# Performance work log

Hardware: AMD Instinct MI355X
Metric: run time of the kernel (lower is better)

The kernel has to match this reference:

```python
import jax, jax.numpy as jnp
import numpy as np

N = 100000
F = 128
H = 128
E = 3200000


def setup_inputs() -> dict:
    key = jax.random.key(0)
    ks = jax.random.split(key, 12)
    s = 1.0 / np.sqrt(F)
    return {
        "x": jax.random.normal(ks[0], (N, F), jnp.float32),
        "edge_weight": jax.random.uniform(ks[1], (E,), jnp.float32),
        "p": jax.random.normal(ks[2], (F,), jnp.float32) * s,
        "w_ih": jax.random.normal(ks[3], (3 * F, F), jnp.float32) * s,
        "w_hh": jax.random.normal(ks[4], (3 * F, F), jnp.float32) * s,
        "b_ih": jax.random.normal(ks[5], (3 * F,), jnp.float32) * s,
        "b_hh": jax.random.normal(ks[6], (3 * F,), jnp.float32) * s,
        "w0": jax.random.normal(ks[7], (F, F), jnp.float32) * s,
        "w_lin": jax.random.normal(ks[8], (H, F), jnp.float32) * s,
        "b_lin": jax.random.normal(ks[9], (H,), jnp.float32) * s,
        "edge_index": jax.random.randint(ks[10], (2, E), 0, N, jnp.int64),
    }


def _evolve_gcnh(x, edge_index, edge_weight, p, w_ih, w_hh, b_ih, b_hh, w0):
    n_nodes, f = x.shape
    # --- TopKPooling: keep k = f nodes by learned projection score ---
    score = jnp.tanh((x @ p) / jnp.linalg.norm(p))  # [N]
    top_scores, idx = jax.lax.top_k(score, f)
    x_tilde = x[idx] * top_scores[:, None]  # [F, F]
    # --- single GRU step (batch=F, input=F): hidden state = GCN weight ---
    gi = x_tilde @ w_ih.T + b_ih  # [F, 3F]
    gh = w0 @ w_hh.T + b_hh       # [F, 3F]
    i_r, i_z, i_n = jnp.split(gi, 3, axis=-1)
    h_r, h_z, h_n = jnp.split(gh, 3, axis=-1)
    r = jax.nn.sigmoid(i_r + h_r)
    z = jax.nn.sigmoid(i_z + h_z)
    n = jnp.tanh(i_n + r * h_n)
    W = (1.0 - z) * n + z * w0  # evolved weight [F, F]
    # --- GCNConv with fixed W: sym-normalized sparse aggregation ---
    src, dst = edge_index[0], edge_index[1]
    loop = jnp.arange(n_nodes)
    src = jnp.concatenate([src, loop])
    dst = jnp.concatenate([dst, loop])
    ew = jnp.concatenate([edge_weight, jnp.ones((n_nodes,), x.dtype)])
    deg = jax.ops.segment_sum(ew, dst, num_segments=n_nodes)
    dinv = jnp.where(deg > 0, jax.lax.rsqrt(deg), 0.0)
    norm = dinv[src] * ew * dinv[dst]  # [E+N]
    xw = x @ W  # [N, F]
    out = jax.ops.segment_sum(norm[:, None] * xw[src], dst, num_segments=n_nodes)
    return out


def reference(x, edge_weight, p, w_ih, w_hh, b_ih, b_hh, w0, w_lin, b_lin, edge_index):
    h = _evolve_gcnh(x, edge_index, edge_weight, p, w_ih, w_hh, b_ih, b_hh, w0)
    h = jax.nn.relu(h)
    return h @ w_lin.T + b_lin
```

## Files before the change

kernel.cpp:

```cpp
#include <hip/hip_runtime.h>
#include <hip/hip_fp16.h>
#include <stdint.h>

#define FD 128
#define CAP 4096
#define PSH 8
#define NPART_MAX 512
#define NBLK1 1024
#define EBUF_MAX 4096

static inline size_t alignup256(size_t x) { return (x + 255) & ~(size_t)255; }

struct EdgeP { int s; float w; };

typedef __attribute__((ext_vector_type(4))) float f32x4;
typedef __attribute__((ext_vector_type(8))) short bf16x8;

__device__ __forceinline__ unsigned short f32_to_bf16(float f) {
  unsigned u = __float_as_uint(f);
  u += 0x7fffu + ((u >> 16) & 1u);
  return (unsigned short)(u >> 16);
}
__device__ __forceinline__ unsigned pack_bf16(float a, float b) {
  return ((unsigned)f32_to_bf16(b) << 16) | (unsigned)f32_to_bf16(a);
}
__device__ __forceinline__ unsigned pack_f16(float a, float b) {
  unsigned short ha = __half_as_ushort(__float2half_rn(a));
  unsigned short hb = __half_as_ushort(__float2half_rn(b));
  return ((unsigned)hb << 16) | (unsigned)ha;
}
__device__ __forceinline__ float f16lo(unsigned u) {
  return __half2float(__ushort_as_half((unsigned short)(u & 0xffffu)));
}
__device__ __forceinline__ float f16hi(unsigned u) {
  return __half2float(__ushort_as_half((unsigned short)(u >> 16)));
}
__device__ __forceinline__ unsigned mono32(float f) {
  unsigned u = __float_as_uint(f);
  return (u & 0x80000000u) ? ~u : (u | 0x80000000u);
}
__device__ __forceinline__ unsigned long long mono64(double d) {
  unsigned long long b = (unsigned long long)__double_as_longlong(d);
  return (b & 0x8000000000000000ULL) ? ~b : (b | 0x8000000000000000ULL);
}

__global__ void score_pack(const float* __restrict__ x, const float* __restrict__ p,
                           double* __restrict__ dvals, unsigned* __restrict__ hist,
                           unsigned short* __restrict__ xb, unsigned* __restrict__ cnt, int N)
{
  int gid = blockIdx.x * blockDim.x + threadIdx.x;
  if (gid == 0) *cnt = 0u;
  int wid = gid >> 6, lane = threadIdx.x & 63;
  int nw = (gridDim.x * blockDim.x) >> 6;
  double p0 = (double)p[lane * 2], p1 = (double)p[lane * 2 + 1];
  for (int n = wid; n < N; n += nw) {
    float2 xv = *(const float2*)(x + (size_t)n * FD + lane * 2);
    unsigned pk = pack_f16(xv.x, xv.y);
    *(unsigned*)(xb + (size_t)n * FD + lane * 2) = pk;
    double s = (double)xv.x * p0 + (double)xv.y * p1;
    #pragma unroll
    for (int o = 32; o > 0; o >>= 1) s += __shfl_down(s, o, 64);
    if (lane == 0) {
      dvals[n] = s;
      unsigned u = mono32((float)s);
      atomicAdd(&hist[u >> 16], 1u);
    }
  }
}

__global__ void find_thresh(const unsigned* __restrict__ hist, unsigned* __restrict__ Bthr)
{
  __shared__ unsigned part[1024];
  int t = threadIdx.x;
  unsigned s = 0;
  for (int i = 0; i < 64; i++) s += hist[t * 64 + i];
  part[t] = s;
  __syncthreads();
  if (t == 0) {
    unsigned cum = 0;
    int chunk = 1023;
    for (; chunk >= 0; chunk--) {
      if (cum + part[chunk] >= 128u) break;
      cum += part[chunk];
    }
    unsigned B = 0;
    if (chunk >= 0) {
      int b = chunk * 64 + 63;
      for (; b >= chunk * 64; b--) {
        cum += hist[b];
        if (cum >= 128u) break;
      }
      B = (unsigned)b;
    }
    *Bthr = B;
  }
}

__global__ void compact_kernel(const double* __restrict__ dvals, const unsigned* __restrict__ Bthr,
                               unsigned long long* __restrict__ ckey, unsigned* __restrict__ cidx,
                               unsigned* __restrict__ cnt, int N)
{
  int i = blockIdx.x * blockDim.x + threadIdx.x;
  if (i >= N) return;
  unsigned B = *Bthr;
  double d = dvals[i];
  unsigned u = mono32((float)d);
  if ((u >> 16) >= B) {
    unsigned pos = atomicAdd(cnt, 1u);
    if (pos < CAP) {
      ckey[pos] = ~mono64(d);
      cidx[pos] = (unsigned)i;
    }
  }
}

__global__ void topk_sort(const double* __restrict__ dvals, const float* __restrict__ p,
                          const unsigned* __restrict__ cnt,
                          const unsigned long long* __restrict__ ckey, const unsigned* __restrict__ cidx,
                          unsigned* __restrict__ sel_idx, float* __restrict__ sel_ts)
{
  __shared__ unsigned long long k[CAP];
  __shared__ unsigned id[CAP];
  __shared__ double red[128];
  __shared__ double pn_sh;
  int t = threadIdx.x;
  unsigned C = *cnt;
  if (C > CAP) C = CAP;
  int S = 128;
  while (S < (int)C) S <<= 1;
  for (int i = t; i < S; i += 1024) {
    if (i < (int)C) { k[i] = ckey[i]; id[i] = cidx[i]; }
    else            { k[i] = ~0ULL;   id[i] = 0xFFFFFFFFu; }
  }
  __syncthreads();
  for (int kk = 2; kk <= S; kk <<= 1) {
    for (int j = kk >> 1; j > 0; j >>= 1) {
      for (int i = t; i < S; i += 1024) {
        int q = i ^ j;
        if (q > i) {
          bool up = ((i & kk) == 0);
          bool g = (k[i] > k[q]) || (k[i] == k[q] && id[i] > id[q]);
          if (g == up) {
            unsigned long long tk = k[i]; k[i] = k[q]; k[q] = tk;
            unsigned ti = id[i]; id[i] = id[q]; id[q] = ti;
          }
        }
      }
      __syncthreads();
    }
  }
  if (t < 128) { double v = (double)p[t]; red[t] = v * v; }
  __syncthreads();
  if (t == 0) {
    double s = 0.0;
    for (int i = 0; i < 128; i++) s += red[i];
    pn_sh = sqrt(s);
  }
  __syncthreads();
  if (t < 128) {
    unsigned n = id[t];
    sel_idx[t] = n;
    sel_ts[t] = (float)tanh(dvals[n] / pn_sh);
  }
}

__global__ void transpose3(const float* __restrict__ w_ih, const float* __restrict__ w_hh,
                           const float* __restrict__ w_lin, float* __restrict__ w_ihT,
                           float* __restrict__ w_hhT, unsigned short* __restrict__ wlb)
{
  int b = blockIdx.x, c = threadIdx.x;
  if (b < 384)      w_ihT[(size_t)c * 384 + b]         = w_ih[(size_t)b * 128 + c];
  else if (b < 768) w_hhT[(size_t)c * 384 + (b - 384)] = w_hh[(size_t)(b - 384) * 128 + c];
  else              wlb[(size_t)(b - 768) * 128 + c]   = f32_to_bf16(w_lin[(size_t)(b - 768) * 128 + c]);
}

__global__ __launch_bounds__(384)
void gru_evolve(const float* __restrict__ x, const unsigned* __restrict__ sel_idx,
                const float* __restrict__ sel_ts,
                const float* __restrict__ w_ihT, const float* __restrict__ w_hhT,
                const float* __restrict__ b_ih, const float* __restrict__ b_hh,
                const float* __restrict__ w0, unsigned short* __restrict__ WbT)
{
  __shared__ float xt[FD], w0r[FD];
  __shared__ float gi[384], gh[384];
  int i = blockIdx.x, j = threadIdx.x;
  if (j < FD) {
    unsigned n = sel_idx[i];
    float ts = sel_ts[i];
    xt[j]  = x[(size_t)n * FD + j] * ts;
    w0r[j] = w0[i * FD + j];
  }
  __syncthreads();
  float gacc = b_ih[j], hacc = b_hh[j];
  for (int kx = 0; kx < FD; kx++) {
    float xv = xt[kx], hv = w0r[kx];
    gacc += xv * w_ihT[(size_t)kx * 384 + j];
    hacc += hv * w_hhT[(size_t)kx * 384 + j];
  }
  gi[j] = gacc;
  gh[j] = hacc;
  __syncthreads();
  if (j < FD) {
    float r = 1.f / (1.f + expf(-(gi[j] + gh[j])));
    float z = 1.f / (1.f + expf(-(gi[128 + j] + gh[128 + j])));
    float nn = tanhf(gi[256 + j] + r * gh[256 + j]);
    float wv = (1.f - z) * nn + z * w0r[j];
    WbT[(size_t)j * FD + i] = f32_to_bf16(wv);
  }
}

__global__ __launch_bounds__(1024)
void part_count(const int* __restrict__ dstA, unsigned* __restrict__ cnt,
                int E, int NPART)
{
  __shared__ unsigned lh[NPART_MAX];
  for (int i = threadIdx.x; i < NPART; i += 1024) lh[i] = 0;
  __syncthreads();
  int chunk = (E + gridDim.x - 1) / gridDim.x;
  int e0 = blockIdx.x * chunk;
  int e1 = e0 + chunk; if (e1 > E) e1 = E;
  for (int e = e0 + threadIdx.x; e < e1; e += 1024)
    atomicAdd(&lh[dstA[e] >> PSH], 1u);
  __syncthreads();
  for (int i = threadIdx.x; i < NPART; i += 1024)
    cnt[(size_t)i * NBLK1 + blockIdx.x] = lh[i];
}

__global__ __launch_bounds__(1024)
void scan_blocks(const unsigned* __restrict__ cnt, unsigned* __restrict__ basel,
                 unsigned* __restrict__ ptot)
{
  __shared__ unsigned s[NBLK1];
  int p = blockIdx.x, t = threadIdx.x;
  unsigned c = cnt[(size_t)p * NBLK1 + t];
  s[t] = c;
  __syncthreads();
  for (int ofs = 1; ofs < NBLK1; ofs <<= 1) {
    unsigned u = (t >= ofs) ? s[t - ofs] : 0u;
    __syncthreads();
    s[t] += u;
    __syncthreads();
  }
  basel[(size_t)p * NBLK1 + t] = s[t] - c;
  if (t == NBLK1 - 1) ptot[p] = s[t];
}

__global__ void scan_parts(const unsigned* __restrict__ ptot, int* __restrict__ poff,
                           int NPART, int E)
{
  __shared__ unsigned s[NPART_MAX];
  int t = threadIdx.x;
  unsigned c = (t < NPART) ? ptot[t] : 0u;
  s[t] = c;
  __syncthreads();
  for (int ofs = 1; ofs < NPART_MAX; ofs <<= 1) {
    unsigned u = (t >= ofs) ? s[t - ofs] : 0u;
    __syncthreads();
    s[t] += u;
    __syncthreads();
  }
  if (t < NPART) poff[t] = (int)(s[t] - c);
  if (t == 0) poff[NPART] = E;
}

__global__ __launch_bounds__(512)
void part_place(const int* __restrict__ srcA, const int* __restrict__ dstA,
                const float* __restrict__ ew, const int* __restrict__ poff,
                const unsigned* __restrict__ basel,
                unsigned long long* __restrict__ epk2, int E, int NPART)
{
  __shared__ unsigned long long ebuf[EBUF_MAX];
  __shared__ unsigned lcnt[NPART_MAX];
  __shared__ unsigned lsc[NPART_MAX];
  __shared__ unsigned lbase[NPART_MAX + 1];
  __shared__ unsigned cur[NPART_MAX];
  __shared__ int gbase[NPART_MAX];
  int b = blockIdx.x, t = threadIdx.x;
  int chunk = (E + gridDim.x - 1) / gridDim.x;
  int e0 = b * chunk;
  int e1 = e0 + chunk; if (e1 > E) e1 = E;
  int n = e1 - e0;

  lcnt[t] = 0;
  __syncthreads();
  for (int e = e0 + t; e < e1; e += 512)
    atomicAdd(&lcnt[dstA[e] >> PSH], 1u);
  __syncthreads();
  lsc[t] = lcnt[t];
  __syncthreads();
  for (int ofs = 1; ofs < NPART_MAX; ofs <<= 1) {
    unsigned u = (t >= ofs) ? lsc[t - ofs] : 0u;
    __syncthreads();
    lsc[t] += u;
    __syncthreads();
  }
  lbase[t] = lsc[t] - lcnt[t];
  if (t == NPART_MAX - 1) lbase[NPART_MAX] = lsc[t];
  cur[t] = lsc[t] - lcnt[t];
  gbase[t] = (t < NPART) ? (poff[t] + (int)basel[(size_t)t * NBLK1 + b]) : 0;
  __syncthreads();
  for (int e = e0 + t; e < e1; e += 512) {
    int d = dstA[e];
    int s = srcA[e];
    float w = ew[e];
    int p = d >> PSH;
    unsigned long long v = ((unsigned long long)__float_as_uint(w) << 32)
                         | ((unsigned long long)(unsigned)s << 8)
                         | (unsigned long long)(d & 255);
    unsigned pos = atomicAdd(&cur[p], 1u);
    ebuf[pos] = v;
  }
  __syncthreads();
  for (int j = t; j < n; j += 512) {
    int lo = 0, hi = NPART_MAX;
    while (hi - lo > 1) {
      int mid = (lo + hi) >> 1;
      if (lbase[mid] <= (unsigned)j) lo = mid; else hi = mid;
    }
    epk2[gbase[lo] + (j - (int)lbase[lo])] = ebuf[j];
  }
}

__global__ void part_csr(const int* __restrict__ poff, const unsigned long long* __restrict__ epk2,
                         EdgeP* __restrict__ epk_out, int* __restrict__ off,
                         float* __restrict__ dinv, int N, int NPART)
{
  int p = blockIdx.x;
  int beg = poff[p], end = poff[p + 1];
  int n0 = p << PSH;
  int nn = N - n0; if (nn > 256) nn = 256;
  __shared__ unsigned lcnt[256];
  __shared__ float ldeg[256];
  __shared__ unsigned lsc[256];
  int t = threadIdx.x;
  lcnt[t] = 0; ldeg[t] = 0.f;
  __syncthreads();
  for (int i = beg + t; i < end; i += 256) {
    unsigned long long v = epk2[i];
    int ln = (int)(v & 255u);
    float w = __uint_as_float((unsigned)(v >> 32));
    atomicAdd(&lcnt[ln], 1u);
    atomicAdd(&ldeg[ln], w);
  }
  __syncthreads();
  unsigned c = lcnt[t];
  lsc[t] = c;
  __syncthreads();
  for (int ofs = 1; ofs < 256; ofs <<= 1) {
    unsigned u = (t >= ofs) ? lsc[t - ofs] : 0u;
    __syncthreads();
    lsc[t] += u;
    __syncthreads();
  }
  unsigned excl = lsc[t] - c;
  if (t < nn) {
    off[n0 + t] = beg + (int)excl;
    dinv[n0 + t] = rsqrtf(ldeg[t] + 1.0f);
  }
  if (p == NPART - 1 && t == 0) off[N] = end;
  lcnt[t] = excl;
  __syncthreads();
  for (int i = beg + t; i < end; i += 256) {
    unsigned long long v = epk2[i];
    int ln = (int)(v & 255u);
    unsigned q = atomicAdd(&lcnt[ln], 1u);
    EdgeP ep;
    ep.s = (int)((v >> 8) & 0xFFFFFFu);
    ep.w = __uint_as_float((unsigned)(v >> 32));
    epk_out[beg + (int)q] = ep;
  }
}

__global__ __launch_bounds__(256)
void csr_gather4(const int* __restrict__ off, const EdgeP* __restrict__ epk,
                 const float* __restrict__ dinv, const unsigned short* __restrict__ xb,
                 unsigned short* __restrict__ aggb, int N)
{
  int gid = blockIdx.x * blockDim.x + threadIdx.x;
  int wid = gid >> 6, lane = threadIdx.x & 63;
  if (wid >= N) return;
  int g = lane >> 4, sub = lane & 15;
  int n = wid;
  int beg = off[n], end = off[n + 1];
  int cnt = end - beg;
  const EdgeP* ep_base = epk + beg;

  float di = dinv[n];
  uint4 xs4 = *(const uint4*)(xb + (size_t)n * FD + sub * 8);

  float acc[8];
  #pragma unroll
  for (int j = 0; j < 8; j++) acc[j] = 0.f;

  int nfull = cnt >> 4;
  int base = 0;
  for (int s16 = 0; s16 < nfull; s16++, base += 16) {
    uint2 ep[4];
    #pragma unroll
    for (int u = 0; u < 4; u++)
      ep[u] = *(const uint2*)(ep_base + base + u * 4 + g);
    float dv[4]; uint4 pv[4];
    #pragma unroll
    for (int u = 0; u < 4; u++) {
      int s = (int)ep[u].x;
      dv[u] = dinv[s];
      pv[u] = *(const uint4*)(xb + (size_t)s * FD + sub * 8);
    }
    #pragma unroll
    for (int u = 0; u < 4; u++) {
      float w = __uint_as_float(ep[u].y) * dv[u];
      acc[0] = fmaf(f16lo(pv[u].x), w, acc[0]); acc[1] = fmaf(f16hi(pv[u].x), w, acc[1]);
      acc[2] = fmaf(f16lo(pv[u].y), w, acc[2]); acc[3] = fmaf(f16hi(pv[u].y), w, acc[3]);
      acc[4] = fmaf(f16lo(pv[u].z), w, acc[4]); acc[5] = fmaf(f16hi(pv[u].z), w, acc[5]);
      acc[6] = fmaf(f16lo(pv[u].w), w, acc[6]); acc[7] = fmaf(f16hi(pv[u].w), w, acc[7]);
    }
  }
  if (base < cnt) {
    int last = cnt - 1;
    uint2 ep[4];
    #pragma unroll
    for (int u = 0; u < 4; u++) {
      int idx = base + u * 4 + g;
      int idc = idx < cnt ? idx : last;
      ep[u] = *(const uint2*)(ep_base + idc);
    }
    float dv[4]; uint4 pv[4];
    #pragma unroll
    for (int u = 0; u < 4; u++) {
      int s = (int)ep[u].x;
      dv[u] = dinv[s];
      pv[u] = *(const uint4*)(xb + (size_t)s * FD + sub * 8);
    }
    #pragma unroll
    for (int u = 0; u < 4; u++) {
      int idx = base + u * 4 + g;
      float w = (idx < cnt) ? __uint_as_float(ep[u].y) * dv[u] : 0.f;
      acc[0] = fmaf(f16lo(pv[u].x), w, acc[0]); acc[1] = fmaf(f16hi(pv[u].x), w, acc[1]);
      acc[2] = fmaf(f16lo(pv[u].y), w, acc[2]); acc[3] = fmaf(f16hi(pv[u].y), w, acc[3]);
      acc[4] = fmaf(f16lo(pv[u].z), w, acc[4]); acc[5] = fmaf(f16hi(pv[u].z), w, acc[5]);
      acc[6] = fmaf(f16lo(pv[u].w), w, acc[6]); acc[7] = fmaf(f16hi(pv[u].w), w, acc[7]);
    }
  }

  #pragma unroll
  for (int j = 0; j < 8; j++) {
    acc[j] += __shfl_xor(acc[j], 16, 64);
    acc[j] += __shfl_xor(acc[j], 32, 64);
  }
  if (g == 0) {
    float dii = di * di;
    uint4 o;
    o.x = pack_bf16(di * acc[0] + dii * f16lo(xs4.x), di * acc[1] + dii * f16hi(xs4.x));
    o.y = pack_bf16(di * acc[2] + dii * f16lo(xs4.y), di * acc[3] + dii * f16hi(xs4.y));
    o.z = pack_bf16(di * acc[4] + dii * f16lo(xs4.z), di * acc[5] + dii * f16hi(xs4.z));
    o.w = pack_bf16(di * acc[6] + dii * f16lo(xs4.w), di * acc[7] + dii * f16hi(xs4.w));
    *(uint4*)(aggb + (size_t)n * FD + sub * 8) = o;
  }
}

__global__ __launch_bounds__(256)
void gemm_mfma(const unsigned short* __restrict__ aggb, const unsigned short* __restrict__ WbT,
               const unsigned short* __restrict__ wlb, const float* __restrict__ bias,
               float* __restrict__ C, int nrows)
{
  __shared__ unsigned short hs[64][136];
  int tid = threadIdx.x;
  int wv = tid >> 6, lane = tid & 63;
  int row16 = lane & 15;
  int kgrp = lane >> 4;
  int r0 = blockIdx.x * 64;
  int arow = r0 + wv * 16 + row16;
  bool rowok = arow < nrows;

  f32x4 acc[8];
  #pragma unroll
  for (int t = 0; t < 8; t++) acc[t] = (f32x4){0.f, 0.f, 0.f, 0.f};

  #pragma unroll
  for (int ks = 0; ks < 4; ks++) {
    int k = ks * 32 + kgrp * 8;
    bf16x8 a;
    if (rowok) a = *(const bf16x8*)(aggb + (size_t)arow * FD + k);
    else       a = (bf16x8){0, 0, 0, 0, 0, 0, 0, 0};
    #pragma unroll
    for (int t = 0; t < 8; t++) {
      int col = t * 16 + row16;
      bf16x8 b = *(const bf16x8*)(WbT + (size_t)col * FD + k);
      acc[t] = __builtin_amdgcn_mfma_f32_16x16x32_bf16(a, b, acc[t], 0, 0, 0);
    }
  }
  #pragma unroll
  for (int t = 0; t < 8; t++) {
    int col = t * 16 + row16;
    #pragma unroll
    for (int r = 0; r < 4; r++) {
      int row_l = wv * 16 + kgrp * 4 + r;
      hs[row_l][col] = f32_to_bf16(fmaxf(acc[t][r], 0.f));
    }
  }
  __syncthreads();

  f32x4 acc2[8];
  #pragma unroll
  for (int t = 0; t < 8; t++) acc2[t] = (f32x4){0.f, 0.f, 0.f, 0.f};
  #pragma unroll
  for (int ks = 0; ks < 4; ks++) {
    int k = ks * 32 + kgrp * 8;
    bf16x8 a = *(const bf16x8*)(&hs[wv * 16 + row16][k]);
    #pragma unroll
    for (int t = 0; t < 8; t++) {
      int col = t * 16 + row16;
      bf16x8 b = *(const bf16x8*)(wlb + (size_t)col * FD + k);
      acc2[t] = __builtin_amdgcn_mfma_f32_16x16x32_bf16(a, b, acc2[t], 0, 0, 0);
    }
  }
  #pragma unroll
  for (int t = 0; t < 8; t++) {
    int col = t * 16 + row16;
    float bl = bias[col];
    #pragma unroll
    for (int r = 0; r < 4; r++) {
      int row = r0 + wv * 16 + kgrp * 4 + r;
      if (row < nrows) C[(size_t)row * FD + col] = acc2[t][r] + bl;
    }
  }
}

extern "C" void kernel_launch(void* const* d_in, const int* in_sizes, int n_in,
                              void* d_out, int out_size, void* d_ws, size_t ws_size,
                              hipStream_t stream)
{
  const float* x     = (const float*)d_in[0];
  const float* ew    = (const float*)d_in[1];
  const float* p     = (const float*)d_in[2];
  const float* w_ih  = (const float*)d_in[3];
  const float* w_hh  = (const float*)d_in[4];
  const float* b_ih  = (const float*)d_in[5];
  const float* b_hh  = (const float*)d_in[6];
  const float* w0    = (const float*)d_in[7];
  const float* w_lin = (const float*)d_in[8];
  const float* b_lin = (const float*)d_in[9];
  const int*   eidx  = (const int*)d_in[10];

  int N = in_sizes[0] / FD;
  int E = in_sizes[1];
  int NPART = (N + 255) >> PSH;
  const int* srcA = eidx;
  const int* dstA = eidx + E;

  char* base = (char*)d_ws;
  size_t off_ws = 0;
  auto take = [&](size_t bytes) -> void* {
    void* ptr = base + off_ws;
    off_ws = alignup256(off_ws + bytes);
    return ptr;
  };
  double* dvals = (double*)take((size_t)N * 8);
  unsigned* hist = (unsigned*)take(65536u * 4);
  unsigned* cnt = (unsigned*)take(4);
  unsigned* Bthr = (unsigned*)take(4);
  unsigned long long* ckey = (unsigned long long*)take((size_t)CAP * 8);
  unsigned* cidx = (unsigned*)take((size_t)CAP * 4);
  unsigned* sel_idx = (unsigned*)take(128 * 4);
  float* sel_ts = (float*)take(128 * 4);
  unsigned short* WbT = (unsigned short*)take(FD * FD * 2);
  unsigned short* wlb = (unsigned short*)take(FD * FD * 2);
  float* w_ihT = (float*)take(3 * FD * FD * 4);
  float* w_hhT = (float*)take(3 * FD * FD * 4);
  float* dinv = (float*)take((size_t)N * 4);
  unsigned* pcnt = (unsigned*)take((size_t)NPART_MAX * NBLK1 * 4);
  unsigned* basel = (unsigned*)take((size_t)NPART_MAX * NBLK1 * 4);
  unsigned* ptot = (unsigned*)take((size_t)NPART_MAX * 4);
  int* poff = (int*)take(((size_t)NPART_MAX + 1) * 4);
  int* off = (int*)take(((size_t)N + 1) * 4);
  unsigned long long* epk2 = (unsigned long long*)take((size_t)E * 8);
  EdgeP* epk_b = (EdgeP*)take((size_t)E * 8);
  unsigned short* xb = (unsigned short*)take((size_t)N * FD * 2);
  unsigned short* aggb = (unsigned short*)take((size_t)N * FD * 2);
  float* out1 = (float*)d_out;

  hipMemsetAsync(hist, 0, 65536u * 4, stream);

  score_pack<<<2048, 256, 0, stream>>>(x, p, dvals, hist, xb, cnt, N);
  find_thresh<<<1, 1024, 0, stream>>>(hist, Bthr);
  compact_kernel<<<(N + 255) / 256, 256, 0, stream>>>(dvals, Bthr, ckey, cidx, cnt, N);
  topk_sort<<<1, 1024, 0, stream>>>(dvals, p, cnt, ckey, cidx, sel_idx, sel_ts);
  transpose3<<<896, 128, 0, stream>>>(w_ih, w_hh, w_lin, w_ihT, w_hhT, wlb);
  gru_evolve<<<128, 384, 0, stream>>>(x, sel_idx, sel_ts, w_ihT, w_hhT, b_ih, b_hh, w0, WbT);

  part_count<<<NBLK1, 1024, 0, stream>>>(dstA, pcnt, E, NPART);
  scan_blocks<<<NPART, NBLK1, 0, stream>>>(pcnt, basel, ptot);
  scan_parts<<<1, NPART_MAX, 0, stream>>>(ptot, poff, NPART, E);
  part_place<<<NBLK1, 512, 0, stream>>>(srcA, dstA, ew, poff, basel, epk2, E, NPART);
  part_csr<<<NPART, 256, 0, stream>>>(poff, epk2, epk_b, off, dinv, N, NPART);

  csr_gather4<<<(N * 64 + 255) / 256, 256, 0, stream>>>(off, epk_b, dinv, xb, aggb, N);
  gemm_mfma<<<(N + 63) / 64, 256, 0, stream>>>(aggb, WbT, wlb, b_lin, out1, N);
}
```

Baseline: 400.4 us.

## Merge independent pipeline stages into shared launches via block-index dispatch

Cuts the launch count from 13 kernels to 6. Independent stages (score/pack, edge partition count, weight transpose; threshold and partition scan; compaction and edge placement; top-k sort and CSR build; GRU and gather) now share one launch each, with blocks routed by block index. The partition offset scan is folded into consumers, which recompute prefix sums of ptot on the fly and drop the poff buffer. The aim is to remove launch gaps and let small serial kernels overlap with large bandwidth-bound ones, at the cost of smaller block sizes for some stages (sort at 256 threads) and redundant prefix sums.

```diff
diff --git a/kernel.cpp b/kernel.cpp
--- a/kernel.cpp
+++ b/kernel.cpp
@@ -8,6 +8,8 @@
 #define NPART_MAX 512
 #define NBLK1 1024
 #define EBUF_MAX 4096
+#define SCORE_BLKS 2048
+#define TRANS_BLKS 448
 
 static inline size_t alignup256(size_t x) { return (x + 255) & ~(size_t)255; }
 
@@ -44,417 +46,425 @@
   return (b & 0x8000000000000000ULL) ? ~b : (b | 0x8000000000000000ULL);
 }
 
-__global__ void score_pack(const float* __restrict__ x, const float* __restrict__ p,
-                           double* __restrict__ dvals, unsigned* __restrict__ hist,
-                           unsigned short* __restrict__ xb, unsigned* __restrict__ cnt, int N)
+__global__ __launch_bounds__(256)
+void k_front(const float* __restrict__ x, const float* __restrict__ pvec,
+             double* __restrict__ dvals, unsigned* __restrict__ hist,
+             unsigned short* __restrict__ xb, unsigned* __restrict__ cnt, int N,
+             const int* __restrict__ dstA, unsigned* __restrict__ pcnt, int E, int NPART,
+             const float* __restrict__ w_ih, const float* __restrict__ w_hh,
+             const float* __restrict__ w_lin, float* __restrict__ w_ihT,
+             float* __restrict__ w_hhT, unsigned short* __restrict__ wlb)
 {
-  int gid = blockIdx.x * blockDim.x + threadIdx.x;
-  if (gid == 0) *cnt = 0u;
-  int wid = gid >> 6, lane = threadIdx.x & 63;
-  int nw = (gridDim.x * blockDim.x) >> 6;
-  double p0 = (double)p[lane * 2], p1 = (double)p[lane * 2 + 1];
-  for (int n = wid; n < N; n += nw) {
-    float2 xv = *(const float2*)(x + (size_t)n * FD + lane * 2);
-    unsigned pk = pack_f16(xv.x, xv.y);
-    *(unsigned*)(xb + (size_t)n * FD + lane * 2) = pk;
-    double s = (double)xv.x * p0 + (double)xv.y * p1;
-    #pragma unroll
-    for (int o = 32; o > 0; o >>= 1) s += __shfl_down(s, o, 64);
-    if (lane == 0) {
-      dvals[n] = s;
-      unsigned u = mono32((float)s);
-      atomicAdd(&hist[u >> 16], 1u);
-    }
-  }
-}
-
-__global__ void find_thresh(const unsigned* __restrict__ hist, unsigned* __restrict__ Bthr)
+  int b = blockIdx.x, t = threadIdx.x;
+  if (b < SCORE_BLKS) {
+    int gid = b * 256 + t;
+    if (gid == 0) *cnt = 0u;
+    int wid = gid >> 6, lane = t & 63;
+    const int nw = (SCORE_BLKS * 256) >> 6;
+    double p0 = (double)pvec[lane * 2], p1 = (double)pvec[lane * 2 + 1];
+    for (int n = wid; n < N; n += nw) {
+      float2 xv = *(const float2*)(x + (size_t)n * FD + lane * 2);
+      unsigned pk = pack_f16(xv.x, xv.y);
+      *(unsigned*)(xb + (size_t)n * FD + lane * 2) = pk;
+      double s = (double)xv.x * p0 + (double)xv.y * p1;
+      #pragma unroll
+      for (int o = 32; o > 0; o >>= 1) s += __shfl_down(s, o, 64);
+      if (lane == 0) {
+        dvals[n] = s;
+        unsigned u = mono32((float)s);
+        atomicAdd(&hist[u >> 16], 1u);
+      }
+    }
+  } else if (b < SCORE_BLKS + NBLK1) {
+    __shared__ unsigned lh[NPART_MAX];
+    int bid = b - SCORE_BLKS;
+    for (int i = t; i < NPART; i += 256) lh[i] = 0;
+    __syncthreads();
+    int chunk = (E + NBLK1 - 1) / NBLK1;
+    int e0 = bid * chunk;
+    int e1 = e0 + chunk; if (e1 > E) e1 = E;
+    for (int e = e0 + t; e < e1; e += 256)
+      atomicAdd(&lh[dstA[e] >> PSH], 1u);
+    __syncthreads();
+    for (int i = t; i < NPART; i += 256)
+      pcnt[(size_t)i * NBLK1 + bid] = lh[i];
+  } else {
+    int vb = (b - SCORE_BLKS - NBLK1) * 2 + (t >> 7);
+    int c = t & 127;
+    if (vb < 384)      w_ihT[(size_t)c * 384 + vb]         = w_ih[(size_t)vb * 128 + c];
+    else if (vb < 768) w_hhT[(size_t)c * 384 + (vb - 384)] = w_hh[(size_t)(vb - 384) * 128 + c];
+    else               wlb[(size_t)(vb - 768) * 128 + c]   = f32_to_bf16(w_lin[(size_t)(vb - 768) * 128 + c]);
+  }
+}
+
+__global__ __launch_bounds__(1024)
+void k_mid1(const unsigned* __restrict__ hist, unsigned* __restrict__ Bthr,
+            const unsigned* __restrict__ pcnt, unsigned* __restrict__ basel,
+            unsigned* __restrict__ ptot)
 {
-  __shared__ unsigned part[1024];
   int t = threadIdx.x;
-  unsigned s = 0;
-  for (int i = 0; i < 64; i++) s += hist[t * 64 + i];
-  part[t] = s;
-  __syncthreads();
-  if (t == 0) {
-    unsigned cum = 0;
-    int chunk = 1023;
-    for (; chunk >= 0; chunk--) {
-      if (cum + part[chunk] >= 128u) break;
-      cum += part[chunk];
-    }
-    unsigned B = 0;
-    if (chunk >= 0) {
-      int b = chunk * 64 + 63;
-      for (; b >= chunk * 64; b--) {
-        cum += hist[b];
-        if (cum >= 128u) break;
-      }
-      B = (unsigned)b;
-    }
-    *Bthr = B;
-  }
-}
-
-__global__ void compact_kernel(const double* __restrict__ dvals, const unsigned* __restrict__ Bthr,
-                               unsigned long long* __restrict__ ckey, unsigned* __restrict__ cidx,
-                               unsigned* __restrict__ cnt, int N)
+  if (blockIdx.x == 0) {
+    __shared__ unsigned part[1024];
+    unsigned s = 0;
+    for (int i = 0; i < 64; i++) s += hist[t * 64 + i];
+    part[t] = s;
+    __syncthreads();
+    if (t == 0) {
+      unsigned cum = 0;
+      int chunk = 1023;
+      for (; chunk >= 0; chunk--) {
+        if (cum + part[chunk] >= 128u) break;
+        cum += part[chunk];
+      }
+      unsigned B = 0;
+      if (chunk >= 0) {
+        int b = chunk * 64 + 63;
+        for (; b >= chunk * 64; b--) {
+          cum += hist[b];
+          if (cum >= 128u) break;
+        }
+        B = (unsigned)b;
+      }
+      *Bthr = B;
+    }
+  } else {
+    __shared__ unsigned s[NBLK1];
+    int p = blockIdx.x - 1;
+    unsigned c = pcnt[(size_t)p * NBLK1 + t];
+    s[t] = c;
+    __syncthreads();
+    for (int ofs = 1; ofs < NBLK1; ofs <<= 1) {
+      unsigned u = (t >= ofs) ? s[t - ofs] : 0u;
+      __syncthreads();
+      s[t] += u;
+      __syncthreads();
+    }
+    basel[(size_t)p * NBLK1 + t] = s[t] - c;
+    if (t == NBLK1 - 1) ptot[p] = s[t];
+  }
+}
+
+__global__ __launch_bounds__(512)
+void k_mid2(const int* __restrict__ srcA, const int* __restrict__ dstA,
+            const float* __restrict__ ew, const unsigned* __restrict__ ptot,
+            const unsigned* __restrict__ basel, unsigned long long* __restrict__ epk2,
+            int E, int NPART,
+            const double* __restrict__ dvals, const unsigned* __restrict__ Bthr,
+            unsigned long long* __restrict__ ckey, unsigned* __restrict__ cidx,
+            unsigned* __restrict__ cnt, int N)
 {
-  int i = blockIdx.x * blockDim.x + threadIdx.x;
-  if (i >= N) return;
-  unsigned B = *Bthr;
-  double d = dvals[i];
-  unsigned u = mono32((float)d);
-  if ((u >> 16) >= B) {
-    unsigned pos = atomicAdd(cnt, 1u);
-    if (pos < CAP) {
-      ckey[pos] = ~mono64(d);
-      cidx[pos] = (unsigned)i;
-    }
-  }
-}
-
-__global__ void topk_sort(const double* __restrict__ dvals, const float* __restrict__ p,
-                          const unsigned* __restrict__ cnt,
-                          const unsigned long long* __restrict__ ckey, const unsigned* __restrict__ cidx,
-                          unsigned* __restrict__ sel_idx, float* __restrict__ sel_ts)
+  int t = threadIdx.x;
+  if (blockIdx.x < NBLK1) {
+    __shared__ unsigned long long ebuf[EBUF_MAX];
+    __shared__ unsigned lcnt[NPART_MAX];
+    __shared__ unsigned lsc[NPART_MAX];
+    __shared__ unsigned psc[NPART_MAX];
+    __shared__ unsigned lbase[NPART_MAX + 1];
+    __shared__ unsigned cur[NPART_MAX];
+    __shared__ int gbase[NPART_MAX];
+    int b = blockIdx.x;
+    int chunk = (E + NBLK1 - 1) / NBLK1;
+    int e0 = b * chunk;
+    int e1 = e0 + chunk; if (e1 > E) e1 = E;
+    int n = e1 - e0;
+
+    lcnt[t] = 0;
+    unsigned pt = (t < NPART) ? ptot[t] : 0u;
+    __syncthreads();
+    for (int e = e0 + t; e < e1; e += 512)
+      atomicAdd(&lcnt[dstA[e] >> PSH], 1u);
+    __syncthreads();
+    lsc[t] = lcnt[t];
+    psc[t] = pt;
+    __syncthreads();
+    for (int ofs = 1; ofs < NPART_MAX; ofs <<= 1) {
+      unsigned u1 = (t >= ofs) ? lsc[t - ofs] : 0u;
+      unsigned u2 = (t >= ofs) ? psc[t - ofs] : 0u;
+      __syncthreads();
+      lsc[t] += u1;
+      psc[t] += u2;
+      __syncthreads();
+    }
+    lbase[t] = lsc[t] - lcnt[t];
+    if (t == NPART_MAX - 1) lbase[NPART_MAX] = lsc[t];
+    cur[t] = lsc[t] - lcnt[t];
+    gbase[t] = (t < NPART) ? ((int)(psc[t] - pt) + (int)basel[(size_t)t * NBLK1 + b]) : 0;
+    __syncthreads();
+    for (int e = e0 + t; e < e1; e += 512) {
+      int d = dstA[e];
+      int s = srcA[e];
+      float w = ew[e];
+      int p = d >> PSH;
+      unsigned long long v = ((unsigned long long)__float_as_uint(w) << 32)
+                           | ((unsigned long long)(unsigned)s << 8)
+                           | (unsigned long long)(d & 255);
+      unsigned pos = atomicAdd(&cur[p], 1u);
+      ebuf[pos] = v;
+    }
+    __syncthreads();
+    for (int j = t; j < n; j += 512) {
+      int lo = 0, hi = NPART_MAX;
+      while (hi - lo > 1) {
+        int mid = (lo + hi) >> 1;
+        if (lbase[mid] <= (unsigned)j) lo = mid; else hi = mid;
+      }
+      epk2[gbase[lo] + (j - (int)lbase[lo])] = ebuf[j];
+    }
+  } else {
+    int i = (blockIdx.x - NBLK1) * 512 + t;
+    if (i >= N) return;
+    unsigned B = *Bthr;
+    double d = dvals[i];
+    unsigned u = mono32((float)d);
+    if ((u >> 16) >= B) {
+      unsigned pos = atomicAdd(cnt, 1u);
+      if (pos < CAP) {
+        ckey[pos] = ~mono64(d);
+        cidx[pos] = (unsigned)i;
+      }
+    }
+  }
+}
+
+__global__ __launch_bounds__(256)
+void k_mid3(const double* __restrict__ dvals, const float* __restrict__ pvec,
+            const unsigned* __restrict__ cnt,
+            const unsigned long long* __restrict__ ckey, const unsigned* __restrict__ cidx,
+            unsigned* __restrict__ sel_idx, float* __restrict__ sel_ts,
+            const unsigned* __restrict__ ptot, const unsigned long long* __restrict__ epk2,
+            EdgeP* __restrict__ epk_out, int* __restrict__ off,
+            float* __restrict__ dinv, int N, int NPART)
 {
-  __shared__ unsigned long long k[CAP];
-  __shared__ unsigned id[CAP];
-  __shared__ double red[128];
-  __shared__ double pn_sh;
   int t = threadIdx.x;
-  unsigned C = *cnt;
-  if (C > CAP) C = CAP;
-  int S = 128;
-  while (S < (int)C) S <<= 1;
-  for (int i = t; i < S; i += 1024) {
-    if (i < (int)C) { k[i] = ckey[i]; id[i] = cidx[i]; }
-    else            { k[i] = ~0ULL;   id[i] = 0xFFFFFFFFu; }
-  }
-  __syncthreads();
-  for (int kk = 2; kk <= S; kk <<= 1) {
-    for (int j = kk >> 1; j > 0; j >>= 1) {
-      for (int i = t; i < S; i += 1024) {
-        int q = i ^ j;
-        if (q > i) {
-          bool up = ((i & kk) == 0);
-          bool g = (k[i] > k[q]) || (k[i] == k[q] && id[i] > id[q]);
-          if (g == up) {
-            unsigned long long tk = k[i]; k[i] = k[q]; k[q] = tk;
-            unsigned ti = id[i]; id[i] = id[q]; id[q] = ti;
+  if (blockIdx.x == 0) {
+    __shared__ unsigned long long k[CAP];
+    __shared__ unsigned id[CAP];
+    __shared__ double red[128];
+    __shared__ double pn_sh;
+    unsigned C = *cnt;
+    if (C > CAP) C = CAP;
+    int S = 128;
+    while (S < (int)C) S <<= 1;
+    for (int i = t; i < S; i += 256) {
+      if (i < (int)C) { k[i] = ckey[i]; id[i] = cidx[i]; }
+      else            { k[i] = ~0ULL;   id[i] = 0xFFFFFFFFu; }
+    }
+    __syncthreads();
+    for (int kk = 2; kk <= S; kk <<= 1) {
+      for (int j = kk >> 1; j > 0; j >>= 1) {
+        for (int i = t; i < S; i += 256) {
+          int q = i ^ j;
+          if (q > i) {
+            bool up = ((i & kk) == 0);
+            bool g = (k[i] > k[q]) || (k[i] == k[q] && id[i] > id[q]);
+            if (g == up) {
+              unsigned long long tk = k[i]; k[i] = k[q]; k[q] = tk;
+              unsigned ti = id[i]; id[i] = id[q]; id[q] = ti;
+            }
           }
         }
-      }
+        __syncthreads();
+      }
+    }
+    if (t < 128) { double v = (double)pvec[t]; red[t] = v * v; }
+    __syncthreads();
+    if (t == 0) {
+      double s = 0.0;
+      for (int i = 0; i < 128; i++) s += red[i];
+      pn_sh = sqrt(s);
+    }
+    __syncthreads();
+    if (t < 128) {
+      unsigned n = id[t];
+      sel_idx[t] = n;
+      sel_ts[t] = (float)tanh(dvals[n] / pn_sh);
+    }
+  } else {
+    int p = blockIdx.x - 1;
+    __shared__ unsigned rsum[256];
+    unsigned a = 0;
+    for (int i = t; i < p; i += 256) a += ptot[i];
+    rsum[t] = a;
+    __syncthreads();
+    for (int ofs = 128; ofs > 0; ofs >>= 1) {
+      if (t < ofs) rsum[t] += rsum[t + ofs];
       __syncthreads();
     }
-  }
-  if (t < 128) { double v = (double)p[t]; red[t] = v * v; }
-  __syncthreads();
-  if (t == 0) {
-    double s = 0.0;
-    for (int i = 0; i < 128; i++) s += red[i];
-    pn_sh = sqrt(s);
-  }
-  __syncthreads();
-  if (t < 128) {
-    unsigned n = id[t];
-    sel_idx[t] = n;
-    sel_ts[t] = (float)tanh(dvals[n] / pn_sh);
-  }
-}
-
-__global__ void transpose3(const float* __restrict__ w_ih, const float* __restrict__ w_hh,
-                           const float* __restrict__ w_lin, float* __restrict__ w_ihT,
-                           float* __restrict__ w_hhT, unsigned short* __restrict__ wlb)
+    int beg = (int)rsum[0];
+    int end = beg + (int)ptot[p];
+
+    int n0 = p << PSH;
+    int nn = N - n0; if (nn > 256) nn = 256;
+    __shared__ unsigned lcnt[256];
+    __shared__ float ldeg[256];
+    __shared__ unsigned lsc[256];
+    lcnt[t] = 0; ldeg[t] = 0.f;
+    __syncthreads();
+    for (int i = beg + t; i < end; i += 256) {
+      unsigned long long v = epk2[i];
+      int ln = (int)(v & 255u);
+      float w = __uint_as_float((unsigned)(v >> 32));
+      atomicAdd(&lcnt[ln], 1u);
+      atomicAdd(&ldeg[ln], w);
+    }
+    __syncthreads();
+    unsigned c = lcnt[t];
+    lsc[t] = c;
+    __syncthreads();
+    for (int ofs = 1; ofs < 256; ofs <<= 1) {
+      unsigned u = (t >= ofs) ? lsc[t - ofs] : 0u;
+      __syncthreads();
+      lsc[t] += u;
+      __syncthreads();
+    }
+    unsigned excl = lsc[t] - c;
+    if (t < nn) {
+      off[n0 + t] = beg + (int)excl;
+      dinv[n0 + t] = rsqrtf(ldeg[t] + 1.0f);
+    }
+    if (p == NPART - 1 && t == 0) off[N] = end;
+    lcnt[t] = excl;
+    __syncthreads();
+    for (int i = beg + t; i < end; i += 256) {
+      unsigned long long v = epk2[i];
+      int ln = (int)(v & 255u);
+      unsigned q = atomicAdd(&lcnt[ln], 1u);
+      EdgeP ep;
+      ep.s = (int)((v >> 8) & 0xFFFFFFu);
+      ep.w = __uint_as_float((unsigned)(v >> 32));
+      epk_out[beg + (int)q] = ep;
+    }
+  }
+}
+
+__global__ __launch_bounds__(256)
+void k_gg(const float* __restrict__ x, const unsigned* __restrict__ sel_idx,
+          const float* __restrict__ sel_ts,
+          const float* __restrict__ w_ihT, const float* __restrict__ w_hhT,
+          const float* __restrict__ b_ih, const float* __restrict__ b_hh,
+          const float* __restrict__ w0, unsigned short* __restrict__ WbT,
+          const int* __restrict__ off, const EdgeP* __restrict__ epk,
+          const float* __restrict__ dinv, const unsigned short* __restrict__ xb,
+          unsigned short* __restrict__ aggb, int N)
 {
-  int b = blockIdx.x, c = threadIdx.x;
-  if (b < 384)      w_ihT[(size_t)c * 384 + b]         = w_ih[(size_t)b * 128 + c];
-  else if (b < 768) w_hhT[(size_t)c * 384 + (b - 384)] = w_hh[(size_t)(b - 384) * 128 + c];
-  else              wlb[(size_t)(b - 768) * 128 + c]   = f32_to_bf16(w_lin[(size_t)(b - 768) * 128 + c]);
-}
-
-__global__ __launch_bounds__(384)
-void gru_evolve(const float* __restrict__ x, const unsigned* __restrict__ sel_idx,
-                const float* __restrict__ sel_ts,
-                const float* __restrict__ w_ihT, const float* __restrict__ w_hhT,
-                const float* __restrict__ b_ih, const float* __restrict__ b_hh,
-                const float* __restrict__ w0, unsigned short* __restrict__ WbT)
-{
-  __shared__ float xt[FD], w0r[FD];
-  __shared__ float gi[384], gh[384];
-  int i = blockIdx.x, j = threadIdx.x;
-  if (j < FD) {
-    unsigned n = sel_idx[i];
-    float ts = sel_ts[i];
-    xt[j]  = x[(size_t)n * FD + j] * ts;
-    w0r[j] = w0[i * FD + j];
-  }
-  __syncthreads();
-  float gacc = b_ih[j], hacc = b_hh[j];
-  for (int kx = 0; kx < FD; kx++) {
-    float xv = xt[kx], hv = w0r[kx];
-    gacc += xv * w_ihT[(size_t)kx * 384 + j];
-    hacc += hv * w_hhT[(size_t)kx * 384 + j];
-  }
-  gi[j] = gacc;
-  gh[j] = hacc;
-  __syncthreads();
-  if (j < FD) {
-    float r = 1.f / (1.f + expf(-(gi[j] + gh[j])));
-    float z = 1.f / (1.f + expf(-(gi[128 + j] + gh[128 + j])));
-    float nn = tanhf(gi[256 + j] + r * gh[256 + j]);
-    float wv = (1.f - z) * nn + z * w0r[j];
-    WbT[(size_t)j * FD + i] = f32_to_bf16(wv);
-  }
-}
-
-__global__ __launch_bounds__(1024)
-void part_count(const int* __restrict__ dstA, unsigned* __restrict__ cnt,
-                int E, int NPART)
-{
-  __shared__ unsigned lh[NPART_MAX];
-  for (int i = threadIdx.x; i < NPART; i += 1024) lh[i] = 0;
-  __syncthreads();
-  int chunk = (E + gridDim.x - 1) / gridDim.x;
-  int e0 = blockIdx.x * chunk;
-  int e1 = e0 + chunk; if (e1 > E) e1 = E;
-  for (int e = e0 + threadIdx.x; e < e1; e += 1024)
-    atomicAdd(&lh[dstA[e] >> PSH], 1u);
-  __syncthreads();
-  for (int i = threadIdx.x; i < NPART; i += 1024)
-    cnt[(size_t)i * NBLK1 + blockIdx.x] = lh[i];
-}
-
-__global__ __launch_bounds__(1024)
-void scan_blocks(const unsigned* __restrict__ cnt, unsigned* __restrict__ basel,
-                 unsigned* __restrict__ ptot)
-{
-  __shared__ unsigned s[NBLK1];
-  int p = blockIdx.x, t = threadIdx.x;
-  unsigned c = cnt[(size_t)p * NBLK1 + t];
-  s[t] = c;
-  __syncthreads();
-  for (int ofs = 1; ofs < NBLK1; ofs <<= 1) {
-    unsigned u = (t >= ofs) ? s[t - ofs] : 0u;
-    __syncthreads();
-    s[t] += u;
-    __syncthreads();
-  }
-  basel[(size_t)p * NBLK1 + t] = s[t] - c;
-  if (t == NBLK1 - 1) ptot[p] = s[t];
-}
-
-__global__ void scan_parts(const unsigned* __restrict__ ptot, int* __restrict__ poff,
-                           int NPART, int E)
-{
-  __shared__ unsigned s[NPART_MAX];
   int t = threadIdx.x;
-  unsigned c = (t < NPART) ? ptot[t] : 0u;
-  s[t] = c;
-  __syncthreads();
-  for (int ofs = 1; ofs < NPART_MAX; ofs <<= 1) {
-    unsigned u = (t >= ofs) ? s[t - ofs] : 0u;
-    __syncthreads();
-    s[t] += u;
-    __syncthreads();
-  }
-  if (t < NPART) poff[t] = (int)(s[t] - c);
-  if (t == 0) poff[NPART] = E;
-}
-
-__global__ __launch_bounds__(512)
-void part_place(const int* __restrict__ srcA, const int* __restrict__ dstA,
-                const float* __restrict__ ew, const int* __restrict__ poff,
-                const unsigned* __restrict__ basel,
-                unsigned long long* __restrict__ epk2, int E, int NPART)
-{
-  __shared__ unsigned long long ebuf[EBUF_MAX];
-  __shared__ unsigned lcnt[NPART_MAX];
-  __shared__ unsigned lsc[NPART_MAX];
-  __shared__ unsigned lbase[NPART_MAX + 1];
-  __shared__ unsigned cur[NPART_MAX];
-  __shared__ int gbase[NPART_MAX];
-  int b = blockIdx.x, t = threadIdx.x;
-  int chunk = (E + gridDim.x - 1) / gridDim.x;
-  int e0 = b * chunk;
-  int e1 = e0 + chunk; if (e1 > E) e1 = E;
-  int n = e1 - e0;
-
-  lcnt[t] = 0;
-  __syncthreads();
-  for (int e = e0 + t; e < e1; e += 512)
-    atomicAdd(&lcnt[dstA[e] >> PSH], 1u);
-  __syncthreads();
-  lsc[t] = lcnt[t];
-  __syncthreads();
-  for (int ofs = 1; ofs < NPART_MAX; ofs <<= 1) {
-    unsigned u = (t >= ofs) ? lsc[t - ofs] : 0u;
-    __syncthreads();
-    lsc[t] += u;
-    __syncthreads();
-  }
-  lbase[t] = lsc[t] - lcnt[t];
-  if (t == NPART_MAX - 1) lbase[NPART_MAX] = lsc[t];
-  cur[t] = lsc[t] - lcnt[t];
-  gbase[t] = (t < NPART) ? (poff[t] + (int)basel[(size_t)t * NBLK1 + b]) : 0;
-  __syncthreads();
-  for (int e = e0 + t; e < e1; e += 512) {
-    int d = dstA[e];
-    int s = srcA[e];
-    float w = ew[e];
-    int p = d >> PSH;
-    unsigned long long v = ((unsigned long long)__float_as_uint(w) << 32)
-                         | ((unsigned long long)(unsigned)s << 8)
-                         | (unsigned long long)(d & 255);
-    unsigned pos = atomicAdd(&cur[p], 1u);
-    ebuf[pos] = v;
-  }
-  __syncthreads();
-  for (int j = t; j < n; j += 512) {
-    int lo = 0, hi = NPART_MAX;
-    while (hi - lo > 1) {
-      int mid = (lo + hi) >> 1;
-      if (lbase[mid] <= (unsigned)j) lo = mid; else hi = mid;
-    }
-    epk2[gbase[lo] + (j - (int)lbase[lo])] = ebuf[j];
-  }
-}
-
-__global__ void part_csr(const int* __restrict__ poff, const unsigned long long* __restrict__ epk2,
-                         EdgeP* __restrict__ epk_out, int* __restrict__ off,
-                         float* __restrict__ dinv, int N, int NPART)
-{
-  int p = blockIdx.x;
-  int beg = poff[p], end = poff[p + 1];
-  int n0 = p << PSH;
-  int nn = N - n0; if (nn > 256) nn = 256;
-  __shared__ unsigned lcnt[256];
-  __shared__ float ldeg[256];
-  __shared__ unsigned lsc[256];
-  int t = threadIdx.x;
-  lcnt[t] = 0; ldeg[t] = 0.f;
-  __syncthreads();
-  for (int i = beg + t; i < end; i += 256) {
-    unsigned long long v = epk2[i];
-    int ln = (int)(v & 255u);
-    float w = __uint_as_float((unsigned)(v >> 32));
-    atomicAdd(&lcnt[ln], 1u);
-    atomicAdd(&ldeg[ln], w);
-  }
-  __syncthreads();
-  unsigned c = lcnt[t];
-  lsc[t] = c;
-  __syncthreads();
-  for (int ofs = 1; ofs < 256; ofs <<= 1) {
-    unsigned u = (t >= ofs) ? lsc[t - ofs] : 0u;
-    __syncthreads();
-    lsc[t] += u;
-    __syncthreads();
-  }
-  unsigned excl = lsc[t] - c;
-  if (t < nn) {
-    off[n0 + t] = beg + (int)excl;
-    dinv[n0 + t] = rsqrtf(ldeg[t] + 1.0f);
-  }
-  if (p == NPART - 1 && t == 0) off[N] = end;
-  lcnt[t] = excl;
-  __syncthreads();
-  for (int i = beg + t; i < end; i += 256) {
-    unsigned long long v = epk2[i];
-    int ln = (int)(v & 255u);
-    unsigned q = atomicAdd(&lcnt[ln], 1u);
-    EdgeP ep;
-    ep.s = (int)((v >> 8) & 0xFFFFFFu);
-    ep.w = __uint_as_float((unsigned)(v >> 32));
-    epk_out[beg + (int)q] = ep;
-  }
-}
-
-__global__ __launch_bounds__(256)
-void csr_gather4(const int* __restrict__ off, const EdgeP* __restrict__ epk,
-                 const float* __restrict__ dinv, const unsigned short* __restrict__ xb,
-                 unsigned short* __restrict__ aggb, int N)
-{
-  int gid = blockIdx.x * blockDim.x + threadIdx.x;
-  int wid = gid >> 6, lane = threadIdx.x & 63;
-  if (wid >= N) return;
-  int g = lane >> 4, sub = lane & 15;
-  int n = wid;
-  int beg = off[n], end = off[n + 1];
-  int cnt = end - beg;
-  const EdgeP* ep_base = epk + beg;
-
-  float di = dinv[n];
-  uint4 xs4 = *(const uint4*)(xb + (size_t)n * FD + sub * 8);
-
-  float acc[8];
-  #pragma unroll
-  for (int j = 0; j < 8; j++) acc[j] = 0.f;
-
-  int nfull = cnt >> 4;
-  int base = 0;
-  for (int s16 = 0; s16 < nfull; s16++, base += 16) {
-    uint2 ep[4];
+  if (blockIdx.x < 128) {
+    __shared__ float xt[FD], w0r[FD];
+    __shared__ float gi[384], gh[384];
+    int i = blockIdx.x;
+    if (t < FD) {
+      unsigned n = sel_idx[i];
+      float ts = sel_ts[i];
+      xt[t]  = x[(size_t)n * FD + t] * ts;
+      w0r[t] = w0[i * FD + t];
+    }
+    __syncthreads();
+    bool has2 = t < 128;
+    float ga0 = b_ih[t], ha0 = b_hh[t];
+    float ga1 = 0.f, ha1 = 0.f;
+    if (has2) { ga1 = b_ih[256 + t]; ha1 = b_hh[256 + t]; }
+    for (int kx = 0; kx < FD; kx++) {
+      float xv = xt[kx], hv = w0r[kx];
+      const float* wi = w_ihT + (size_t)kx * 384;
+      const float* wh = w_hhT + (size_t)kx * 384;
+      ga0 += xv * wi[t];
+      ha0 += hv * wh[t];
+      if (has2) {
+        ga1 += xv * wi[256 + t];
+        ha1 += hv * wh[256 + t];
+      }
+    }
+    gi[t] = ga0; gh[t] = ha0;
+    if (has2) { gi[256 + t] = ga1; gh[256 + t] = ha1; }
+    __syncthreads();
+    if (t < FD) {
+      float r = 1.f / (1.f + expf(-(gi[t] + gh[t])));
+      float z = 1.f / (1.f + expf(-(gi[128 + t] + gh[128 + t])));
+      float nn = tanhf(gi[256 + t] + r * gh[256 + t]);
+      float wv = (1.f - z) * nn + z * w0r[t];
+      WbT[(size_t)t * FD + i] = f32_to_bf16(wv);
+    }
+  } else {
+    int gid = (blockIdx.x - 128) * 256 + t;
+    int wid = gid >> 6, lane = t & 63;
+    if (wid >= N) return;
+    int g = lane >> 4, sub = lane & 15;
+    int n = wid;
+    int beg = off[n], end = off[n + 1];
+    int cnt = end - beg;
+    const EdgeP* ep_base = epk + beg;
+
+    float di = dinv[n];
+    uint4 xs4 = *(const uint4*)(xb + (size_t)n * FD + sub * 8);
+
+    float acc[8];
     #pragma unroll
-    for (int u = 0; u < 4; u++)
-      ep[u] = *(const uint2*)(ep_base + base + u * 4 + g);
-    float dv[4]; uint4 pv[4];
+    for (int j = 0; j < 8; j++) acc[j] = 0.f;
+
+    int nfull = cnt >> 4;
+    int base = 0;
+    for (int s16 = 0; s16 < nfull; s16++, base += 16) {
+      uint2 ep[4];
+      #pragma unroll
+      for (int u = 0; u < 4; u++)
+        ep[u] = *(const uint2*)(ep_base + base + u * 4 + g);
+      float dv[4]; uint4 pv[4];
+      #pragma unroll
+      for (int u = 0; u < 4; u++) {
+        int s = (int)ep[u].x;
+        dv[u] = dinv[s];
+        pv[u] = *(const uint4*)(xb + (size_t)s * FD + sub * 8);
+      }
+      #pragma unroll
+      for (int u = 0; u < 4; u++) {
+        float w = __uint_as_float(ep[u].y) * dv[u];
+        acc[0] = fmaf(f16lo(pv[u].x), w, acc[0]); acc[1] = fmaf(f16hi(pv[u].x), w, acc[1]);
+        acc[2] = fmaf(f16lo(pv[u].y), w, acc[2]); acc[3] = fmaf(f16hi(pv[u].y), w, acc[3]);
+        acc[4] = fmaf(f16lo(pv[u].z), w, acc[4]); acc[5] = fmaf(f16hi(pv[u].z), w, acc[5]);
+        acc[6] = fmaf(f16lo(pv[u].w), w, acc[6]); acc[7] = fmaf(f16hi(pv[u].w), w, acc[7]);
+      }
+    }
+    if (base < cnt) {
+      int last = cnt - 1;
+      uint2 ep[4];
+      #pragma unroll
+      for (int u = 0; u < 4; u++) {
+        int idx = base + u * 4 + g;
+        int idc = idx < cnt ? idx : last;
+        ep[u] = *(const uint2*)(ep_base + idc);
+      }
+      float dv[4]; uint4 pv[4];
+      #pragma unroll
+      for (int u = 0; u < 4; u++) {
+        int s = (int)ep[u].x;
+        dv[u] = dinv[s];
+        pv[u] = *(const uint4*)(xb + (size_t)s * FD + sub * 8);
+      }
+      #pragma unroll
+      for (int u = 0; u < 4; u++) {
+        int idx = base + u * 4 + g;
+        float w = (idx < cnt) ? __uint_as_float(ep[u].y) * dv[u] : 0.f;
+        acc[0] = fmaf(f16lo(pv[u].x), w, acc[0]); acc[1] = fmaf(f16hi(pv[u].x), w, acc[1]);
+        acc[2] = fmaf(f16lo(pv[u].y), w, acc[2]); acc[3] = fmaf(f16hi(pv[u].y), w, acc[3]);
+        acc[4] = fmaf(f16lo(pv[u].z), w, acc[4]); acc[5] = fmaf(f16hi(pv[u].z), w, acc[5]);
+        acc[6] = fmaf(f16lo(pv[u].w), w, acc[6]); acc[7] = fmaf(f16hi(pv[u].w), w, acc[7]);
+      }
+    }
+
     #pragma unroll
-    for (int u = 0; u < 4; u++) {
-      int s = (int)ep[u].x;
-      dv[u] = dinv[s];
-      pv[u] = *(const uint4*)(xb + (size_t)s * FD + sub * 8);
-    }
-    #pragma unroll
-    for (int u = 0; u < 4; u++) {
-      float w = __uint_as_float(ep[u].y) * dv[u];
-      acc[0] = fmaf(f16lo(pv[u].x), w, acc[0]); acc[1] = fmaf(f16hi(pv[u].x), w, acc[1]);
-      acc[2] = fmaf(f16lo(pv[u].y), w, acc[2]); acc[3] = fmaf(f16hi(pv[u].y), w, acc[3]);
-      acc[4] = fmaf(f16lo(pv[u].z), w, acc[4]); acc[5] = fmaf(f16hi(pv[u].z), w, acc[5]);
-      acc[6] = fmaf(f16lo(pv[u].w), w, acc[6]); acc[7] = fmaf(f16hi(pv[u].w), w, acc[7]);
-    }
-  }
-  if (base < cnt) {
-    int last = cnt - 1;
-    uint2 ep[4];
-    #pragma unroll
-    for (int u = 0; u < 4; u++) {
-      int idx = base + u * 4 + g;
-      int idc = idx < cnt ? idx : last;
-      ep[u] = *(const uint2*)(ep_base + idc);
-    }
-    float dv[4]; uint4 pv[4];
-    #pragma unroll
-    for (int u = 0; u < 4; u++) {
-      int s = (int)ep[u].x;
-      dv[u] = dinv[s];
-      pv[u] = *(const uint4*)(xb + (size_t)s * FD + sub * 8);
-    }
-    #pragma unroll
-    for (int u = 0; u < 4; u++) {
-      int idx = base + u * 4 + g;
-      float w = (idx < cnt) ? __uint_as_float(ep[u].y) * dv[u] : 0.f;
-      acc[0] = fmaf(f16lo(pv[u].x), w, acc[0]); acc[1] = fmaf(f16hi(pv[u].x), w, acc[1]);
-      acc[2] = fmaf(f16lo(pv[u].y), w, acc[2]); acc[3] = fmaf(f16hi(pv[u].y), w, acc[3]);
-      acc[4] = fmaf(f16lo(pv[u].z), w, acc[4]); acc[5] = fmaf(f16hi(pv[u].z), w, acc[5]);
-      acc[6] = fmaf(f16lo(pv[u].w), w, acc[6]); acc[7] = fmaf(f16hi(pv[u].w), w, acc[7]);
-    }
-  }
-
-  #pragma unroll
-  for (int j = 0; j < 8; j++) {
-    acc[j] += __shfl_xor(acc[j], 16, 64);
-    acc[j] += __shfl_xor(acc[j], 32, 64);
-  }
-  if (g == 0) {
-    float dii = di * di;
-    uint4 o;
-    o.x = pack_bf16(di * acc[0] + dii * f16lo(xs4.x), di * acc[1] + dii * f16hi(xs4.x));
-    o.y = pack_bf16(di * acc[2] + dii * f16lo(xs4.y), di * acc[3] + dii * f16hi(xs4.y));
-    o.z = pack_bf16(di * acc[4] + dii * f16lo(xs4.z), di * acc[5] + dii * f16hi(xs4.z));
-    o.w = pack_bf16(di * acc[6] + dii * f16lo(xs4.w), di * acc[7] + dii * f16hi(xs4.w));
-    *(uint4*)(aggb + (size_t)n * FD + sub * 8) = o;
+    for (int j = 0; j < 8; j++) {
+      acc[j] += __shfl_xor(acc[j], 16, 64);
+      acc[j] += __shfl_xor(acc[j], 32, 64);
+    }
+    if (g == 0) {
+      float dii = di * di;
+      uint4 o;
+      o.x = pack_bf16(di * acc[0] + dii * f16lo(xs4.x), di * acc[1] + dii * f16hi(xs4.x));
+      o.y = pack_bf16(di * acc[2] + dii * f16lo(xs4.y), di * acc[3] + dii * f16hi(xs4.y));
+      o.z = pack_bf16(di * acc[4] + dii * f16lo(xs4.z), di * acc[5] + dii * f16hi(xs4.z));
+      o.w = pack_bf16(di * acc[6] + dii * f16lo(xs4.w), di * acc[7] + dii * f16hi(xs4.w));
+      *(uint4*)(aggb + (size_t)n * FD + sub * 8) = o;
+    }
   }
 }
 
@@ -532,7 +542,7 @@
 {
   const float* x     = (const float*)d_in[0];
   const float* ew    = (const float*)d_in[1];
-  const float* p     = (const float*)d_in[2];
+  const float* pvec  = (const float*)d_in[2];
   const float* w_ih  = (const float*)d_in[3];
   const float* w_hh  = (const float*)d_in[4];
   const float* b_ih  = (const float*)d_in[5];
@@ -571,7 +581,6 @@
   unsigned* pcnt = (unsigned*)take((size_t)NPART_MAX * NBLK1 * 4);
   unsigned* basel = (unsigned*)take((size_t)NPART_MAX * NBLK1 * 4);
   unsigned* ptot = (unsigned*)take((size_t)NPART_MAX * 4);
-  int* poff = (int*)take(((size_t)NPART_MAX + 1) * 4);
   int* off = (int*)take(((size_t)N + 1) * 4);
   unsigned long long* epk2 = (unsigned long long*)take((size_t)E * 8);
   EdgeP* epk_b = (EdgeP*)take((size_t)E * 8);
@@ -581,19 +590,18 @@
 
   hipMemsetAsync(hist, 0, 65536u * 4, stream);
 
-  score_pack<<<2048, 256, 0, stream>>>(x, p, dvals, hist, xb, cnt, N);
-  find_thresh<<<1, 1024, 0, stream>>>(hist, Bthr);
-  compact_kernel<<<(N + 255) / 256, 256, 0, stream>>>(dvals, Bthr, ckey, cidx, cnt, N);
-  topk_sort<<<1, 1024, 0, stream>>>(dvals, p, cnt, ckey, cidx, sel_idx, sel_ts);
-  transpose3<<<896, 128, 0, stream>>>(w_ih, w_hh, w_lin, w_ihT, w_hhT, wlb);
-  gru_evolve<<<128, 384, 0, stream>>>(x, sel_idx, sel_ts, w_ihT, w_hhT, b_ih, b_hh, w0, WbT);
-
-  part_count<<<NBLK1, 1024, 0, stream>>>(dstA, pcnt, E, NPART);
-  scan_blocks<<<NPART, NBLK1, 0, stream>>>(pcnt, basel, ptot);
-  scan_parts<<<1, NPART_MAX, 0, stream>>>(ptot, poff, NPART, E);
-  part_place<<<NBLK1, 512, 0, stream>>>(srcA, dstA, ew, poff, basel, epk2, E, NPART);
-  part_csr<<<NPART, 256, 0, stream>>>(poff, epk2, epk_b, off, dinv, N, NPART);
-
-  csr_gather4<<<(N * 64 + 255) / 256, 256, 0, stream>>>(off, epk_b, dinv, xb, aggb, N);
+  k_front<<<SCORE_BLKS + NBLK1 + TRANS_BLKS, 256, 0, stream>>>(
+      x, pvec, dvals, hist, xb, cnt, N, dstA, pcnt, E, NPART,
+      w_ih, w_hh, w_lin, w_ihT, w_hhT, wlb);
+  k_mid1<<<1 + NPART, 1024, 0, stream>>>(hist, Bthr, pcnt, basel, ptot);
+  k_mid2<<<NBLK1 + (N + 511) / 512, 512, 0, stream>>>(
+      srcA, dstA, ew, ptot, basel, epk2, E, NPART,
+      dvals, Bthr, ckey, cidx, cnt, N);
+  k_mid3<<<1 + NPART, 256, 0, stream>>>(
+      dvals, pvec, cnt, ckey, cidx, sel_idx, sel_ts,
+      ptot, epk2, epk_b, off, dinv, N, NPART);
+  k_gg<<<128 + (N * 64 + 255) / 256, 256, 0, stream>>>(
+      x, sel_idx, sel_ts, w_ihT, w_hhT, b_ih, b_hh, w0, WbT,
+      off, epk_b, dinv, xb, aggb, N);
   gemm_mfma<<<(N + 63) / 64, 256, 0, stream>>>(aggb, WbT, wlb, b_lin, out1, N);
 }
```

Result: faster. 364.8 us (-8.9%).
